# Optimization experiments

Hardware: AMD Instinct MI355X
Metric: run time of the kernel (lower is better)

The kernel has to match this reference:

```python
import jax, jax.numpy as jnp
import numpy as np
from jax import lax

# Module config (matches init_kwargs): mode='swta', patchwise=True, w_nrm=True, k=1, alpha=1
COUT, CIN, KH, KW = 32, 16, 3, 3
STRIDE = 1
K_TEMP = 1.0


def setup_inputs() -> dict:
    key = jax.random.key(0)
    k1, k2 = jax.random.split(key)
    x = jax.random.normal(k1, (16, CIN, 256, 256), dtype=jnp.float32)
    # xavier_normal_: std = sqrt(2/(fan_in+fan_out)), fan_in=CIN*KH*KW, fan_out=COUT*KH*KW
    std = float(np.sqrt(2.0 / (CIN * KH * KW + COUT * KH * KW)))
    weight = jax.random.normal(k2, (COUT, CIN, KH, KW), dtype=jnp.float32) * std
    bias = jnp.zeros((COUT,), dtype=jnp.float32)
    return {"x": x, "weight": weight, "bias": bias}


def _unfold(x, kh, kw, sh, sw):
    # torch F.unfold: output [B, C*kh*kw, L], patch features ordered (c, kh, kw)
    B, C, H, W = x.shape
    Ho = (H - kh) // sh + 1
    Wo = (W - kw) // sw + 1
    cols = [x[:, :, i:i + (Ho - 1) * sh + 1:sh, j:j + (Wo - 1) * sw + 1:sw]
            for i in range(kh) for j in range(kw)]  # each [B,C,Ho,Wo]
    p = jnp.stack(cols, axis=2)  # [B, C, kh*kw, Ho, Wo]
    return p.reshape(B, C * kh * kw, Ho * Wo)


def reference(x, weight, bias):
    # --- compute_activation: weight-normalized conv2d (act = Identity) ---
    nrm = jnp.sqrt((weight ** 2).sum(axis=(1, 2, 3), keepdims=True))
    nrm = jnp.where(nrm == 0, jnp.ones_like(nrm), nrm)
    w = weight / nrm
    y = lax.conv_general_dilated(
        x, w, window_strides=(STRIDE, STRIDE), padding='VALID',
        dimension_numbers=('NCHW', 'OIHW', 'NCHW')) + bias[None, :, None, None]

    # --- SWTA Hebbian update (torch: under no_grad, stored into delta_w buffer) ---
    x_unf = _unfold(x, KH, KW, STRIDE, STRIDE)               # [B, CKK, L]
    x_flat = x_unf.transpose(0, 2, 1).reshape(-1, x_unf.shape[1])  # [B*L, CKK]
    r = jax.nn.softmax(y * K_TEMP, axis=1).transpose(1, 0, 2, 3)   # [O, B, Ho, Wo]
    r_sum = jnp.abs(r).sum(axis=(1, 2, 3), keepdims=True)
    r_sum = jnp.where(r_sum == 0, jnp.ones_like(r_sum), r_sum)
    cr = (jnp.abs(r) / r_sum) * r                             # [O, B, Ho, Wo]
    cr_flat = cr.reshape(COUT, -1)                            # [O, B*L]
    dec = cr_flat.sum(axis=1, keepdims=True) * weight.reshape(COUT, -1)
    delta_w = (cr_flat @ x_flat - dec).reshape(weight.shape)  # [O, CIN, KH, KW]

    return y, delta_w
```

## Files before the change

### kernel.cpp

```cpp
#include <hip/hip_runtime.h>


typedef unsigned short ushort_t;
typedef __attribute__((ext_vector_type(8)))  short  short8v;
typedef __attribute__((ext_vector_type(4)))  float  float4v;
typedef __attribute__((ext_vector_type(16))) float  float16v;

struct __attribute__((packed, aligned(4))) f4a { float x,y,z,w; };
struct __attribute__((packed, aligned(2))) u2a { ushort_t x,y; };

#define BATCH 16
#define CIN   16
#define H     256
#define W     256
#define HW    (H*W)
#define OCH   32
#define HO    254
#define WO    254
#define LPOS  (HO*WO)
#define YELEMS (BATCH*OCH*LPOS)
#define KFEAT 144
#define NROWS (BATCH*HO)
#define NCHUNK (NROWS*8)
#define GRIDA 1016
#define NSLAB GRIDA
#define NGRP  8
#define SLABS_PER_GRP 127

#define TCOLS 36

#define WS_RSUM 0
#define WS_R2   32
#define WS_ACC  64
#define WS_MODE 4672
#define WS_WNB  4680
#define WS_PART 8192
#define WS_PART2 (8192 + NSLAB*4608)
#define WS_NEED ((size_t)(WS_PART2 + NGRP*4608)*4)

__device__ __forceinline__ float bf2f(ushort_t u){
  union{unsigned u; float f;} c; c.u = ((unsigned)u) << 16; return c.f;
}
__device__ __forceinline__ ushort_t f2bf(float f){
  union{float f; unsigned u;} c; c.f = f;
  unsigned x = c.u;
  return (ushort_t)((x + 0x7fffu + ((x >> 16) & 1u)) >> 16);
}
__device__ __forceinline__ unsigned as_u(float f){
  union{float f; unsigned u;} c; c.f = f; return c.u;
}
__device__ __forceinline__ void gload_lds16(const float* g, void* l){
  __builtin_amdgcn_global_load_lds(
      (const __attribute__((address_space(1))) void*)g,
      (__attribute__((address_space(3))) void*)l, 16, 0, 0);
}

__global__ __launch_bounds__(256) void hebb_prep(const ushort_t* __restrict__ x,
                                                 const ushort_t* __restrict__ w,
                                                 int* __restrict__ mode,
                                                 float* __restrict__ ws){
  int tid = threadIdx.x;
  int bad = 0;
  for (int i = tid; i < 16384; i += 256){
    unsigned e = ((unsigned)x[i] >> 7) & 0xFFu;
    bad |= (e >= 0x8Cu) ? 1 : 0;
  }
  unsigned long long m = __ballot(bad);
  __shared__ unsigned long long sm[4];
  __shared__ int mode_s;
  __shared__ float w_s[4608];
  __shared__ float inv_s[OCH];
  int wv = tid >> 6;
  if ((tid & 63) == 0) sm[wv] = m;
  __syncthreads();
  if (tid == 0){
    int md = ((sm[0] | sm[1] | sm[2] | sm[3]) != 0ULL) ? 1 : 0;
    *mode = md; mode_s = md;
  }
  __syncthreads();
  const int fp32 = mode_s;
  const float* wf = (const float*)w;
  for (int i = tid; i < 4608; i += 256)
    w_s[i] = fp32 ? wf[i] : bf2f(w[i]);
  __syncthreads();
  {
    int o = tid >> 3, part = tid & 7;
    float s = 0.f;
    int k0 = part*18;
    for (int k = k0; k < k0+18; k++){ float v = w_s[o*KFEAT + k]; s += v*v; }
    s += __shfl_xor(s, 1); s += __shfl_xor(s, 2); s += __shfl_xor(s, 4);
    if (part == 0){
      float nrm = sqrtf(s);
      inv_s[o] = (nrm == 0.f) ? 1.f : (1.f/nrm);
    }
  }
  __syncthreads();
  ushort_t* wnb = (ushort_t*)(ws + WS_WNB);
  for (int i = tid; i < 4608; i += 256){
    int o = i & 31, rest = i >> 5;
    int ij = rest >> 4, c = rest & 15;
    int k = c*9 + ij;
    wnb[i] = f2bf(w_s[o*KFEAT + k] * inv_s[o]);
    ws[WS_ACC + i] = 0.f;
  }
  if (tid < 64) ws[WS_RSUM + tid] = 0.f;
}

template<int FP32>
__global__ __launch_bounds__(256, 2) void hebb_passAB(
    const void* __restrict__ xv_, const void* __restrict__ bias_,
    const int* __restrict__ mode, const float* __restrict__ ws,
    float* __restrict__ rsum_g, float* __restrict__ r2sum_g,
    void* __restrict__ yout_, float* __restrict__ partial, int do_hebb){
  if (*mode != FP32) return;
  __shared__ __align__(16) float xtile[4][1792];
  __shared__ __align__(16) ushort_t r2t[4][32*40];
  __shared__ float red_s[64];
  float* redp = &xtile[0][0];
  int tid = threadIdx.x;
  if (tid < 64) red_s[tid] = 0.f;
  __syncthreads();
  int wave = tid >> 6, lane = tid & 63;
  int pos = lane & 31, half = lane >> 5;
  int quad = lane >> 4, l16 = lane & 15;

  int bid = (int)blockIdx.x;
  int swz = (bid & 7)*127 + (bid >> 3);

  const ushort_t* wnb = (const ushort_t*)(ws + WS_WNB);
  short8v wa[9];
  #pragma unroll
  for (int ij = 0; ij < 9; ij++){
    union{ushort_t s[8]; short8v v;} pk;
    #pragma unroll
    for (int i = 0; i < 8; i++)
      pk.s[i] = wnb[(ij*16 + half*8 + i)*32 + pos];
    wa[ij] = pk.v;
  }
  float bv[16];
  #pragma unroll
  for (int r = 0; r < 16; r++){
    int och = (r&3) + 8*(r>>2) + 4*half;
    bv[r] = FP32 ? ((const float*)bias_)[och] : bf2f(((const ushort_t*)bias_)[och]);
  }
  float rsA[16];
  #pragma unroll
  for (int r = 0; r < 16; r++) rsA[r] = 0.f;
  float r2B0 = 0.f, r2B1 = 0.f;

  int goff[7], qcol[7];
  #pragma unroll
  for (int i = 0; i < 7; i++){
    int slot = i*64 + lane; slot = (slot > 431) ? 431 : slot;
    int rr = slot/9, q = slot - 9*rr;
    int c = rr/3, ii = rr - 3*c;
    goff[i] = c*HW + ii*W;
    qcol[i] = q*4;
  }

  float4v hacc[18];
  #pragma unroll
  for (int i = 0; i < 18; i++) hacc[i] = (float4v){0.f,0.f,0.f,0.f};

  ushort_t* t2 = r2t[wave];
  float* tw = &xtile[wave][0];

  for (int cc0 = swz*4 + wave; cc0 < NCHUNK; cc0 += GRIDA*4){
    int cc = __builtin_amdgcn_readfirstlane(cc0);
    int row = cc >> 3, sub = cc & 7;
    int b = row / HO, ho = row - b*HO;
    int wo0 = sub << 5;
    int wo = wo0 + pos;
    int tail = (sub == 7);

    float16v av;
    #pragma unroll
    for (int r = 0; r < 16; r++) av[r] = bv[r];

    if (FP32){
      const float* xb = (const float*)xv_ + (size_t)b*(CIN*HW) + (size_t)ho*W;
      #pragma unroll
      for (int i = 0; i < 7; i++){
        int col = wo0 + qcol[i]; col = (col > 252) ? 252 : col;
        gload_lds16(xb + goff[i] + col, (char*)tw + i*1024);
      }
      asm volatile("s_waitcnt vmcnt(0)" ::: "memory");

      #pragma unroll
      for (int ij = 0; ij < 9; ij++){
        const int ii = ij/3, jj = ij - 3*ii;
        unsigned g[8];
        #pragma unroll
        for (int i2 = 0; i2 < 8; i2++)
          g[i2] = as_u(tw[((half*8 + i2)*3 + ii)*TCOLS + pos + jj]) + 0x8000u;
        union{unsigned u[4]; short8v v;} pk;
        pk.u[0] = __builtin_amdgcn_perm(g[1], g[0], 0x07060302u);
        pk.u[1] = __builtin_amdgcn_perm(g[3], g[2], 0x07060302u);
        pk.u[2] = __builtin_amdgcn_perm(g[5], g[4], 0x07060302u);
        pk.u[3] = __builtin_amdgcn_perm(g[7], g[6], 0x07060302u);
        av = __builtin_amdgcn_mfma_f32_32x32x16_bf16(wa[ij], pk.v, av, 0, 0, 0);
      }
    } else {
      #pragma unroll
      for (int ij = 0; ij < 9; ij++){
        const int ii = ij/3, jj = ij - 3*ii;
        int wcol = wo + jj; wcol = (wcol < 256) ? wcol : 255;
        size_t a0 = (size_t)b*(CIN*HW) + (size_t)(half*8)*HW + (size_t)(ho+ii)*W + wcol;
        const ushort_t* xp = (const ushort_t*)xv_;
        union{ushort_t s[8]; short8v v;} pk;
        #pragma unroll
        for (int i2 = 0; i2 < 8; i2++)
          pk.s[i2] = xp[a0 + (size_t)i2*HW];
        av = __builtin_amdgcn_mfma_f32_32x32x16_bf16(wa[ij], pk.v, av, 0, 0, 0);
      }
    }

    int valid = (wo < WO) ? 1 : 0;
    if (valid){
      size_t yb = (size_t)b*(OCH*(size_t)LPOS) + (size_t)(half*4)*LPOS
                + (size_t)ho*WO + wo;
      #pragma unroll
      for (int r = 0; r < 16; r++){
        size_t yi = yb + (size_t)(((r&3) + 8*(r>>2)))*LPOS;
        if (FP32) ((float*)yout_)[yi] = av[r];
        else      ((ushort_t*)yout_)[yi] = f2bf(av[r]);
      }
    }

    float m = -3.0e38f;
    #pragma unroll
    for (int r = 0; r < 16; r++) m = fmaxf(m, av[r]);
    m = fmaxf(m, __shfl_xor(m, 32));
    float s = 0.f;
    #pragma unroll
    for (int r = 0; r < 16; r++){ float e = __expf(av[r] - m); av[r] = e; s += e; }
    s += __shfl_xor(s, 32);
    float inv = valid ? (1.f/s) : 0.f;

    #pragma unroll
    for (int r = 0; r < 16; r++){
      float rr = av[r]*inv;
      rsA[r] += rr;
      int och = (r&3) + 8*(r>>2) + 4*half;
      t2[och*40 + pos] = f2bf(rr*rr);
    }

    short8v a0 = *(const short8v*)(t2 + l16*40      + quad*8);
    short8v a1 = *(const short8v*)(t2 + (16+l16)*40 + quad*8);
    {
      float p0 = 0.f, p1 = 0.f;
      #pragma unroll
      for (int i = 0; i < 8; i++){
        p0 += bf2f((ushort_t)a0[i]);
        p1 += bf2f((ushort_t)a1[i]);
      }
      r2B0 += p0; r2B1 += p1;
    }

    if (do_hebb){
      __builtin_amdgcn_s_setprio(1);
      if (FP32){
        #pragma unroll
        for (int n = 0; n < 9; n++){
          int kh = n*16 + l16, c = kh/9, ij2 = kh - 9*c, ii = ij2/3, jj = ij2 - 3*ii;
          const float* hp = tw + (c*3 + ii)*TCOLS + jj + quad*8;
          unsigned f[8];
          #pragma unroll
          for (int i = 0; i < 8; i++) f[i] = as_u(hp[i]);
          union{unsigned u[4]; short8v v;} pk;
          pk.u[0] = __builtin_amdgcn_perm(f[1], f[0], 0x07060302u);
          pk.u[1] = __builtin_amdgcn_perm(f[3], f[2], 0x07060302u);
          pk.u[2] = __builtin_amdgcn_perm(f[5], f[4], 0x07060302u);
          pk.u[3] = __builtin_amdgcn_perm(f[7], f[6], 0x07060302u);
          hacc[n]   = __builtin_amdgcn_mfma_f32_16x16x32_bf16(a0, pk.v, hacc[n],   0,0,0);
          hacc[9+n] = __builtin_amdgcn_mfma_f32_16x16x32_bf16(a1, pk.v, hacc[9+n], 0,0,0);
        }
      } else {
        int xbase = b*(CIN*HW) + ho*W + wo0;
        #pragma unroll
        for (int n = 0; n < 9; n++){
          int kh = n*16 + l16, c = kh/9, ij2 = kh - 9*c, ii = ij2/3, jj = ij2 - 3*ii;
          int ko = (c*H + ii)*W + jj;
          const ushort_t* xp = (const ushort_t*)xv_ + (size_t)(xbase + ko + quad*8);
          union{ushort_t s[8]; short8v v;} pk;
          if (tail && quad == 3){
            u2a u0 = *(const u2a*)xp, u1 = *(const u2a*)(xp+2), u2 = *(const u2a*)(xp+4);
            pk.s[0]=u0.x; pk.s[1]=u0.y; pk.s[2]=u1.x; pk.s[3]=u1.y;
            pk.s[4]=u2.x; pk.s[5]=u2.y; pk.s[6]=0; pk.s[7]=0;
          } else {
            u2a u0 = *(const u2a*)xp,   u1 = *(const u2a*)(xp+2);
            u2a u2 = *(const u2a*)(xp+4), u3 = *(const u2a*)(xp+6);
            pk.s[0]=u0.x; pk.s[1]=u0.y; pk.s[2]=u1.x; pk.s[3]=u1.y;
            pk.s[4]=u2.x; pk.s[5]=u2.y; pk.s[6]=u3.x; pk.s[7]=u3.y;
          }
          hacc[n]   = __builtin_amdgcn_mfma_f32_16x16x32_bf16(a0, pk.v, hacc[n],   0,0,0);
          hacc[9+n] = __builtin_amdgcn_mfma_f32_16x16x32_bf16(a1, pk.v, hacc[9+n], 0,0,0);
        }
      }
      __builtin_amdgcn_s_setprio(0);
    }
  }

  #pragma unroll
  for (int r = 0; r < 16; r++){
    float a = rsA[r];
    #pragma unroll
    for (int off = 1; off < 32; off <<= 1)
      a += __shfl_xor(a, off);
    if (pos == 0){
      int och = (r&3) + 8*(r>>2) + 4*half;
      atomicAdd(&red_s[och], a);
    }
  }
  r2B0 += __shfl_xor(r2B0, 16); r2B0 += __shfl_xor(r2B0, 32);
  r2B1 += __shfl_xor(r2B1, 16); r2B1 += __shfl_xor(r2B1, 32);
  if (lane < 16){
    atomicAdd(&red_s[32 + lane],      r2B0);
    atomicAdd(&red_s[32 + 16 + lane], r2B1);
  }
  __syncthreads();
  if (tid < 32)      atomicAdd(rsum_g  + tid,      red_s[tid]);
  else if (tid < 64) atomicAdd(r2sum_g + (tid-32), red_s[tid]);

  if (do_hebb){
    for (int wv = 0; wv < 4; wv++){
      if (wave == wv){
        #pragma unroll
        for (int mi = 0; mi < 2; mi++)
          #pragma unroll
          for (int n = 0; n < 9; n++)
            #pragma unroll
            for (int rg = 0; rg < 4; rg++){
              int o  = mi*16 + quad*4 + rg;
              int kh = n*16 + l16;
              if (wv == 0) redp[o*KFEAT + kh]  = hacc[mi*9+n][rg];
              else         redp[o*KFEAT + kh] += hacc[mi*9+n][rg];
            }
      }
      __syncthreads();
    }
    float* myp = partial + (size_t)blockIdx.x*4608;
    for (int i = tid; i < 4608; i += 256) myp[i] = redp[i];
  }
}

__global__ __launch_bounds__(256) void hebb_red(const float* __restrict__ partial,
                                                float* __restrict__ partial2){
  int t = blockIdx.x*256 + threadIdx.x;
  if (t >= NGRP*4608) return;
  int g = t / 4608, col = t - g*4608;
  const float* p = partial + (size_t)g*SLABS_PER_GRP*4608 + col;
  float s0=0.f, s1=0.f, s2=0.f, s3=0.f;
  int j = 0;
  for (; j + 4 <= SLABS_PER_GRP; j += 4){
    s0 += p[(size_t)(j  )*4608];
    s1 += p[(size_t)(j+1)*4608];
    s2 += p[(size_t)(j+2)*4608];
    s3 += p[(size_t)(j+3)*4608];
  }
  for (; j < SLABS_PER_GRP; j++) s0 += p[(size_t)j*4608];
  partial2[t] = ((s0+s1)+(s2+s3));
}

template<int FP32>
__global__ __launch_bounds__(256) void hebb_passB_fb(
    const void* __restrict__ xv_, const int* __restrict__ mode,
    const float* __restrict__ ws, const void* __restrict__ ybf_,
    float* __restrict__ acc_g){
  if (*mode != FP32) return;
  __shared__ __align__(16) ushort_t crs[32*128];
  __shared__ __align__(16) ushort_t xs[144*128];
  __shared__ float rsinv_s[32];
  int tid = threadIdx.x;
  if (tid < 32){
    float rs = ws[WS_RSUM + tid];
    rsinv_s[tid] = (rs == 0.f) ? 1.f : (1.f/rs);
  }
  __syncthreads();

  float4v av[18];
  #pragma unroll
  for (int i = 0; i < 18; i++) av[i] = (float4v){0.f,0.f,0.f,0.f};
  int wave = tid >> 6, lane = tid & 63;
  int quad = lane >> 4, l16 = lane & 15;
  int t = tid & 127, kh0 = tid >> 7;

  for (int s = blockIdx.x; s < NROWS*2; s += (int)gridDim.x){
    int row = s >> 1, half = s & 1;
    int b = row / HO, ho = row - b*HO;
    int wo0 = half << 7;
    int tlen = half ? (WO - 128) : 128;
    size_t xoff = (size_t)b*(CIN*HW) + (size_t)ho*W + wo0;
    bool tvalid = t < tlen;

    #pragma unroll
    for (int it = 0; it < 72; it++){
      const int kh = 2*it + kh0;
      const int c = kh/9, ij = kh - 9*c, ii = ij/3, jj = ij - 3*ii;
      size_t gi = xoff + (size_t)(c*H + ii)*W + jj + t;
      ushort_t val;
      if (FP32) val = tvalid ? f2bf(((const float*)xv_)[gi]) : (ushort_t)0;
      else      val = tvalid ? ((const ushort_t*)xv_)[gi]    : (ushort_t)0;
      xs[kh*128 + t] = val;
    }
    if (tid < 128){
      if (tvalid){
        float r[32];
        size_t yb = (size_t)b*(OCH*(size_t)LPOS) + (size_t)ho*WO + wo0 + tid;
        float m = -3.0e38f;
        #pragma unroll
        for (int o = 0; o < 32; o++){
          float v = FP32 ? ((const float*)ybf_)[yb + (size_t)o*LPOS]
                         : bf2f(((const ushort_t*)ybf_)[yb + (size_t)o*LPOS]);
          r[o] = v; m = fmaxf(m, v);
        }
        float ssum = 0.f;
        #pragma unroll
        for (int o = 0; o < 32; o++){ r[o] = __expf(r[o]-m); ssum += r[o]; }
        float inv = 1.f/ssum;
        #pragma unroll
        for (int o = 0; o < 32; o++) r[o] *= inv;
        #pragma unroll
        for (int o = 0; o < 32; o++) crs[o*128 + tid] = f2bf(r[o]*r[o]*rsinv_s[o]);
      } else {
        #pragma unroll
        for (int o = 0; o < 32; o++) crs[o*128 + tid] = 0;
      }
    }
    __syncthreads();

    int t0 = wave*32;
    short8v a0 = *(const short8v*)(crs + l16*128      + t0 + quad*8);
    short8v a1 = *(const short8v*)(crs + (16+l16)*128 + t0 + quad*8);
    #pragma unroll
    for (int n = 0; n < 9; n++){
      short8v bfr = *(const short8v*)(xs + (n*16 + l16)*128 + t0 + quad*8);
      av[n]   = __builtin_amdgcn_mfma_f32_16x16x32_bf16(a0, bfr, av[n],   0,0,0);
      av[9+n] = __builtin_amdgcn_mfma_f32_16x16x32_bf16(a1, bfr, av[9+n], 0,0,0);
    }
    __syncthreads();
  }

  #pragma unroll
  for (int mi = 0; mi < 2; mi++)
    #pragma unroll
    for (int n = 0; n < 9; n++)
      #pragma unroll
      for (int rg = 0; rg < 4; rg++){
        int o  = mi*16 + quad*4 + rg;
        int kh = n*16 + l16;
        atomicAdd(acc_g + o*KFEAT + kh, av[mi*9+n][rg]);
      }
}

__global__ __launch_bounds__(256) void hebb_fin(const ushort_t* __restrict__ w,
    const int* __restrict__ mode, const float* __restrict__ ws,
    const float* __restrict__ partial2, int use_rbuf, void* __restrict__ dout){
  int tid = blockIdx.x*256 + threadIdx.x;
  if (tid >= 4608) return;
  const int fp32 = *mode;
  int o = tid / KFEAT;
  float rs = ws[WS_RSUM + o];
  rs = (rs == 0.f) ? 1.f : rs;
  float base;
  if (use_rbuf){
    float s = 0.f;
    #pragma unroll
    for (int j = 0; j < NGRP; j++)
      s += partial2[(size_t)j*4608 + tid];
    base = s / rs;
  } else {
    base = ws[WS_ACC + tid];
  }
  float crsum = ws[WS_R2 + o] / rs;
  float wv = fp32 ? ((const float*)w)[tid] : bf2f(w[tid]);
  float d = base - crsum * wv;
  if (fp32) ((float*)dout)[(size_t)YELEMS + tid] = d;
  else      ((ushort_t*)dout)[(size_t)YELEMS + tid] = f2bf(d);
}

extern "C" void kernel_launch(void* const* d_in, const int* in_sizes, int n_in,
                              void* d_out, int out_size, void* d_ws, size_t ws_size,
                              hipStream_t stream){
  const void* x    = d_in[0];
  const ushort_t* w = (const ushort_t*)d_in[1];
  const void* bias = d_in[2];
  float* ws   = (float*)d_ws;
  int*   mode = (int*)(ws + WS_MODE);
  float* part = ws + WS_PART;
  float* part2 = ws + WS_PART2;
  int use_rbuf = (ws_size >= WS_NEED) ? 1 : 0;

  hebb_prep<<<1, 256, 0, stream>>>((const ushort_t*)x, w, mode, ws);
  hebb_passAB<0><<<GRIDA, 256, 0, stream>>>(x, bias, mode, ws,
                                            ws + WS_RSUM, ws + WS_R2, d_out,
                                            part, use_rbuf);
  hebb_passAB<1><<<GRIDA, 256, 0, stream>>>(x, bias, mode, ws,
                                            ws + WS_RSUM, ws + WS_R2, d_out,
                                            part, use_rbuf);
  if (use_rbuf){
    hebb_red<<<144, 256, 0, stream>>>(part, part2);
  } else {
    hebb_passB_fb<0><<<512, 256, 0, stream>>>(x, mode, ws, d_out, ws + WS_ACC);
    hebb_passB_fb<1><<<512, 256, 0, stream>>>(x, mode, ws, d_out, ws + WS_ACC);
  }
  hebb_fin<<<18, 256, 0, stream>>>(w, mode, ws, part2, use_rbuf, d_out);
}
```

Before: 281.2 us.

## Fold prep kernel into main pass and route channel sums through partial slabs

Removes the single-block prep kernel on the default path. Each main-pass block now detects the input dtype itself, normalises the weights into LDS, and stores its per-channel softmax sums in an extended partial slab instead of issuing global atomics. The reduction and final kernels then sum these extra slab entries. This avoids a serialized launch and the atomic contention, but every one of the 1016 blocks now redoes a 16K-element dtype scan and the weight normalisation, which adds redundant work per block.

Measured after the change: 288.8 us. 1.03x slower.

```diff
diff --git a/kernel.cpp b/kernel.cpp
--- a/kernel.cpp
+++ b/kernel.cpp
@@ -26,6 +26,7 @@
 #define NSLAB GRIDA
 #define NGRP  8
 #define SLABS_PER_GRP 127
+#define SLABW 4672
 
 #define TCOLS 36
 
@@ -35,8 +36,8 @@
 #define WS_MODE 4672
 #define WS_WNB  4680
 #define WS_PART 8192
-#define WS_PART2 (8192 + NSLAB*4608)
-#define WS_NEED ((size_t)(WS_PART2 + NGRP*4608)*4)
+#define WS_PART2 (8192 + NSLAB*SLABW)
+#define WS_NEED ((size_t)(WS_PART2 + NGRP*SLABW)*4)
 
 __device__ __forceinline__ float bf2f(ushort_t u){
   union{unsigned u; float f;} c; c.u = ((unsigned)u) << 16; return c.f;
@@ -68,8 +69,6 @@
   unsigned long long m = __ballot(bad);
   __shared__ unsigned long long sm[4];
   __shared__ int mode_s;
-  __shared__ float w_s[4608];
-  __shared__ float inv_s[OCH];
   int wv = tid >> 6;
   if ((tid & 63) == 0) sm[wv] = m;
   __syncthreads();
@@ -80,6 +79,8 @@
   __syncthreads();
   const int fp32 = mode_s;
   const float* wf = (const float*)w;
+  __shared__ float w_s[4608];
+  __shared__ float inv_s[OCH];
   for (int i = tid; i < 4608; i += 256)
     w_s[i] = fp32 ? wf[i] : bf2f(w[i]);
   __syncthreads();
@@ -95,48 +96,88 @@
     }
   }
   __syncthreads();
-  ushort_t* wnb = (ushort_t*)(ws + WS_WNB);
+  for (int i = tid; i < 4608; i += 256)
+    ws[WS_ACC + i] = 0.f;
+  if (tid < 64) ws[WS_RSUM + tid] = 0.f;
+}
+
+template<int FP32>
+__global__ __launch_bounds__(256, 2) void hebb_passAB(
+    const void* __restrict__ xv_, const ushort_t* __restrict__ w_,
+    const void* __restrict__ bias_,
+    int* __restrict__ mode_p, const float* __restrict__ ws,
+    float* __restrict__ rsum_g, float* __restrict__ r2sum_g,
+    void* __restrict__ yout_, float* __restrict__ partial, int do_hebb){
+  __shared__ __align__(16) float xtile[4][1792];
+  __shared__ __align__(16) ushort_t r2t[4][32*40];
+  __shared__ float red_s[64];
+  __shared__ float inv_s[OCH];
+  __shared__ unsigned long long sm4[4];
+  __shared__ int mode_sh;
+  float* redp = &xtile[0][0];
+  int tid = threadIdx.x;
+
+  {
+    const ushort_t* xs16 = (const ushort_t*)xv_;
+    int bad = 0;
+    for (int i = tid; i < 16384; i += 256){
+      unsigned e = ((unsigned)xs16[i] >> 7) & 0xFFu;
+      bad |= (e >= 0x8Cu) ? 1 : 0;
+    }
+    unsigned long long mb = __ballot(bad);
+    if ((tid & 63) == 0) sm4[tid >> 6] = mb;
+    __syncthreads();
+    if (tid == 0) mode_sh = ((sm4[0]|sm4[1]|sm4[2]|sm4[3]) != 0ULL) ? 1 : 0;
+    __syncthreads();
+  }
+  if (mode_sh != FP32) return;
+  if (tid == 0) *mode_p = FP32;
+
+  if (tid < 64) red_s[tid] = 0.f;
+  int wave = tid >> 6, lane = tid & 63;
+  int pos = lane & 31, half = lane >> 5;
+  int quad = lane >> 4, l16 = lane & 15;
+
+  float* wsc = &xtile[0][0];
+  {
+    const float* wf = (const float*)w_;
+    for (int i = tid; i < 4608; i += 256)
+      wsc[i] = FP32 ? wf[i] : bf2f(w_[i]);
+    __syncthreads();
+    int o = tid >> 3, part = tid & 7;
+    float s = 0.f;
+    int k0 = part*18;
+    for (int k = k0; k < k0+18; k++){ float v = wsc[o*KFEAT + k]; s += v*v; }
+    s += __shfl_xor(s, 1); s += __shfl_xor(s, 2); s += __shfl_xor(s, 4);
+    if (part == 0){
+      float nrm = sqrtf(s);
+      inv_s[o] = (nrm == 0.f) ? 1.f : (1.f/nrm);
+    }
+    __syncthreads();
+  }
+  ushort_t* wnb_l = &r2t[0][0];
   for (int i = tid; i < 4608; i += 256){
     int o = i & 31, rest = i >> 5;
     int ij = rest >> 4, c = rest & 15;
     int k = c*9 + ij;
-    wnb[i] = f2bf(w_s[o*KFEAT + k] * inv_s[o]);
-    ws[WS_ACC + i] = 0.f;
-  }
-  if (tid < 64) ws[WS_RSUM + tid] = 0.f;
-}
-
-template<int FP32>
-__global__ __launch_bounds__(256, 2) void hebb_passAB(
-    const void* __restrict__ xv_, const void* __restrict__ bias_,
-    const int* __restrict__ mode, const float* __restrict__ ws,
-    float* __restrict__ rsum_g, float* __restrict__ r2sum_g,
-    void* __restrict__ yout_, float* __restrict__ partial, int do_hebb){
-  if (*mode != FP32) return;
-  __shared__ __align__(16) float xtile[4][1792];
-  __shared__ __align__(16) ushort_t r2t[4][32*40];
-  __shared__ float red_s[64];
-  float* redp = &xtile[0][0];
-  int tid = threadIdx.x;
-  if (tid < 64) red_s[tid] = 0.f;
-  __syncthreads();
-  int wave = tid >> 6, lane = tid & 63;
-  int pos = lane & 31, half = lane >> 5;
-  int quad = lane >> 4, l16 = lane & 15;
+    wnb_l[i] = f2bf(wsc[o*KFEAT + k] * inv_s[o]);
+  }
+  __syncthreads();
+
+  short8v wa[9];
+  #pragma unroll
+  for (int ij = 0; ij < 9; ij++){
+    union{ushort_t s[8]; short8v v;} pk;
+    #pragma unroll
+    for (int i = 0; i < 8; i++)
+      pk.s[i] = wnb_l[(ij*16 + half*8 + i)*32 + pos];
+    wa[ij] = pk.v;
+  }
+  __syncthreads();
 
   int bid = (int)blockIdx.x;
   int swz = (bid & 7)*127 + (bid >> 3);
 
-  const ushort_t* wnb = (const ushort_t*)(ws + WS_WNB);
-  short8v wa[9];
-  #pragma unroll
-  for (int ij = 0; ij < 9; ij++){
-    union{ushort_t s[8]; short8v v;} pk;
-    #pragma unroll
-    for (int i = 0; i < 8; i++)
-      pk.s[i] = wnb[(ij*16 + half*8 + i)*32 + pos];
-    wa[ij] = pk.v;
-  }
   float bv[16];
   #pragma unroll
   for (int r = 0; r < 16; r++){
@@ -319,10 +360,10 @@
     atomicAdd(&red_s[32 + 16 + lane], r2B1);
   }
   __syncthreads();
-  if (tid < 32)      atomicAdd(rsum_g  + tid,      red_s[tid]);
-  else if (tid < 64) atomicAdd(r2sum_g + (tid-32), red_s[tid]);
-
+
+  float* myp = partial + (size_t)blockIdx.x*SLABW;
   if (do_hebb){
+    if (tid < 64) myp[4608 + tid] = red_s[tid];
     for (int wv = 0; wv < 4; wv++){
       if (wave == wv){
         #pragma unroll
@@ -339,26 +380,28 @@
       }
       __syncthreads();
     }
-    float* myp = partial + (size_t)blockIdx.x*4608;
     for (int i = tid; i < 4608; i += 256) myp[i] = redp[i];
+  } else {
+    if (tid < 32)      atomicAdd(rsum_g  + tid,      red_s[tid]);
+    else if (tid < 64) atomicAdd(r2sum_g + (tid-32), red_s[tid]);
   }
 }
 
 __global__ __launch_bounds__(256) void hebb_red(const float* __restrict__ partial,
                                                 float* __restrict__ partial2){
   int t = blockIdx.x*256 + threadIdx.x;
-  if (t >= NGRP*4608) return;
-  int g = t / 4608, col = t - g*4608;
-  const float* p = partial + (size_t)g*SLABS_PER_GRP*4608 + col;
+  if (t >= NGRP*SLABW) return;
+  int g = t / SLABW, col = t - g*SLABW;
+  const float* p = partial + (size_t)g*SLABS_PER_GRP*SLABW + col;
   float s0=0.f, s1=0.f, s2=0.f, s3=0.f;
   int j = 0;
   for (; j + 4 <= SLABS_PER_GRP; j += 4){
-    s0 += p[(size_t)(j  )*4608];
-    s1 += p[(size_t)(j+1)*4608];
-    s2 += p[(size_t)(j+2)*4608];
-    s3 += p[(size_t)(j+3)*4608];
-  }
-  for (; j < SLABS_PER_GRP; j++) s0 += p[(size_t)j*4608];
+    s0 += p[(size_t)(j  )*SLABW];
+    s1 += p[(size_t)(j+1)*SLABW];
+    s2 += p[(size_t)(j+2)*SLABW];
+    s3 += p[(size_t)(j+3)*SLABW];
+  }
+  for (; j < SLABS_PER_GRP; j++) s0 += p[(size_t)j*SLABW];
   partial2[t] = ((s0+s1)+(s2+s3));
 }
 
@@ -460,19 +503,23 @@
   if (tid >= 4608) return;
   const int fp32 = *mode;
   int o = tid / KFEAT;
-  float rs = ws[WS_RSUM + o];
+  float rs, r2, base_raw;
+  if (use_rbuf){
+    rs = 0.f; r2 = 0.f; base_raw = 0.f;
+    #pragma unroll
+    for (int j = 0; j < NGRP; j++){
+      base_raw += partial2[(size_t)j*SLABW + tid];
+      rs       += partial2[(size_t)j*SLABW + 4608 + o];
+      r2       += partial2[(size_t)j*SLABW + 4640 + o];
+    }
+  } else {
+    rs = ws[WS_RSUM + o];
+    r2 = ws[WS_R2 + o];
+    base_raw = 0.f;
+  }
   rs = (rs == 0.f) ? 1.f : rs;
-  float base;
-  if (use_rbuf){
-    float s = 0.f;
-    #pragma unroll
-    for (int j = 0; j < NGRP; j++)
-      s += partial2[(size_t)j*4608 + tid];
-    base = s / rs;
-  } else {
-    base = ws[WS_ACC + tid];
-  }
-  float crsum = ws[WS_R2 + o] / rs;
+  float base = use_rbuf ? (base_raw / rs) : ws[WS_ACC + tid];
+  float crsum = r2 / rs;
   float wv = fp32 ? ((const float*)w)[tid] : bf2f(w[tid]);
   float d = base - crsum * wv;
   if (fp32) ((float*)dout)[(size_t)YELEMS + tid] = d;
@@ -491,16 +538,22 @@
   float* part2 = ws + WS_PART2;
   int use_rbuf = (ws_size >= WS_NEED) ? 1 : 0;
 
-  hebb_prep<<<1, 256, 0, stream>>>((const ushort_t*)x, w, mode, ws);
-  hebb_passAB<0><<<GRIDA, 256, 0, stream>>>(x, bias, mode, ws,
-                                            ws + WS_RSUM, ws + WS_R2, d_out,
-                                            part, use_rbuf);
-  hebb_passAB<1><<<GRIDA, 256, 0, stream>>>(x, bias, mode, ws,
-                                            ws + WS_RSUM, ws + WS_R2, d_out,
-                                            part, use_rbuf);
   if (use_rbuf){
-    hebb_red<<<144, 256, 0, stream>>>(part, part2);
+    hebb_passAB<1><<<GRIDA, 256, 0, stream>>>(x, w, bias, mode, ws,
+                                              ws + WS_RSUM, ws + WS_R2, d_out,
+                                              part, 1);
+    hebb_passAB<0><<<GRIDA, 256, 0, stream>>>(x, w, bias, mode, ws,
+                                              ws + WS_RSUM, ws + WS_R2, d_out,
+                                              part, 1);
+    hebb_red<<<146, 256, 0, stream>>>(part, part2);
   } else {
+    hebb_prep<<<1, 256, 0, stream>>>((const ushort_t*)x, w, mode, ws);
+    hebb_passAB<1><<<GRIDA, 256, 0, stream>>>(x, w, bias, mode, ws,
+                                              ws + WS_RSUM, ws + WS_R2, d_out,
+                                              part, 0);
+    hebb_passAB<0><<<GRIDA, 256, 0, stream>>>(x, w, bias, mode, ws,
+                                              ws + WS_RSUM, ws + WS_R2, d_out,
+                                              part, 0);
     hebb_passB_fb<0><<<512, 256, 0, stream>>>(x, mode, ws, d_out, ws + WS_ACC);
     hebb_passB_fb<1><<<512, 256, 0, stream>>>(x, mode, ws, d_out, ws + WS_ACC);
   }
```
